# Optimization experiments

Measured on AMD Instinct MI355X. Metric: run time of the kernel, lower is better.

## Reference

```python
import jax, jax.numpy as jnp
import numpy as np

DIM = 512
EXPAND = 2
D_INNER = DIM * EXPAND            # 1024
HEADDIM = DIM * EXPAND // 8       # 128
NHEADS = D_INNER // HEADDIM       # 8
D_STATE = 128
D_CONV = 4
CONV_DIM = D_INNER + 2 * D_STATE  # 1280 (x, B, C channels)
D_IN_PROJ = 2 * D_INNER + 2 * D_STATE + NHEADS  # 2312
BSZ = 4
IMG = (16, 16, 16)                # 4096 tokens


def setup_inputs() -> dict:
    key = jax.random.key(0)
    ks = jax.random.split(key, 8)
    x = jax.random.normal(ks[0], (BSZ, DIM, *IMG), jnp.float32)
    in_proj_w = jax.random.normal(ks[1], (D_IN_PROJ, DIM), jnp.float32) * (DIM ** -0.5)
    conv_w = jax.random.normal(ks[2], (CONV_DIM, D_CONV), jnp.float32) * 0.3
    conv_b = jax.random.normal(ks[3], (CONV_DIM,), jnp.float32) * 0.1
    dt_bias = jax.random.normal(ks[4], (NHEADS,), jnp.float32) * 0.5
    A_log = jnp.log(jnp.arange(1, NHEADS + 1, dtype=jnp.float32))
    D_param = jnp.ones((NHEADS,), jnp.float32) + 0.1 * jax.random.normal(ks[5], (NHEADS,), jnp.float32)
    norm_w = jnp.ones((D_INNER,), jnp.float32)
    out_proj_w = jax.random.normal(ks[6], (DIM, D_INNER), jnp.float32) * (D_INNER ** -0.5)
    return dict(x=x, in_proj_w=in_proj_w, conv_w=conv_w, conv_b=conv_b,
                dt_bias=dt_bias, A_log=A_log, D_param=D_param,
                norm_w=norm_w, out_proj_w=out_proj_w)


def reference(x, in_proj_w, conv_w, conv_b, dt_bias, A_log, D_param, norm_w, out_proj_w):
    Bsz, C = x.shape[:2]
    img_dims = x.shape[2:]
    u = x.reshape(Bsz, C, -1).transpose(0, 2, 1)          # [b, L, d_model]
    L = u.shape[1]

    zxbcdt = jnp.einsum('bld,ed->ble', u, in_proj_w)      # [b, L, 2312]
    z = zxbcdt[..., :D_INNER]                             # gate
    xBC = zxbcdt[..., D_INNER:D_INNER + CONV_DIM]
    dt = zxbcdt[..., D_INNER + CONV_DIM:]                 # [b, L, h]
    dt = jax.nn.softplus(dt + dt_bias)

    # causal depthwise conv1d (kernel 4) + SiLU
    xp = jnp.pad(xBC, ((0, 0), (D_CONV - 1, 0), (0, 0)))
    conv = conv_b + sum(xp[:, k:k + L, :] * conv_w[:, k] for k in range(D_CONV))
    xBC = jax.nn.silu(conv)

    xs = xBC[..., :D_INNER].reshape(Bsz, L, NHEADS, HEADDIM)   # [b, L, h, p]
    Bmat = xBC[..., D_INNER:D_INNER + D_STATE]                 # [b, L, n] (ngroups=1)
    Cmat = xBC[..., D_INNER + D_STATE:]                        # [b, L, n]

    A = -jnp.exp(A_log)                                        # [h]
    dA = jnp.exp(dt * A)                                       # [b, L, h]

    def step(state, inp):
        # state: [b, h, p, n]
        x_t, B_t, C_t, dA_t, dt_t = inp
        state = state * dA_t[:, :, None, None] + \
                jnp.einsum('bhp,bn->bhpn', dt_t[:, :, None] * x_t, B_t)
        y_t = jnp.einsum('bhpn,bn->bhp', state, C_t)
        return state, y_t

    init = jnp.zeros((Bsz, NHEADS, HEADDIM, D_STATE), x.dtype)
    inputs = (xs.transpose(1, 0, 2, 3), Bmat.transpose(1, 0, 2),
              Cmat.transpose(1, 0, 2), dA.transpose(1, 0, 2), dt.transpose(1, 0, 2))
    _, ys = jax.lax.scan(step, init, inputs)                   # ys: [L, b, h, p]

    y = ys.transpose(1, 0, 2, 3) + D_param[None, None, :, None] * xs
    y = y.reshape(Bsz, L, D_INNER)

    # gated RMSNorm (norm_before_gate=False): rmsnorm(y * silu(z)) * w
    y = y * jax.nn.silu(z)
    y = y * jax.lax.rsqrt(jnp.mean(y * y, axis=-1, keepdims=True) + 1e-5) * norm_w

    out = jnp.einsum('ble,de->bld', y, out_proj_w)             # [b, L, d_model]
    out = out.transpose(0, 2, 1).reshape(Bsz, C, *img_dims)
    return out + x
```

## Files before the change

kernel.cpp:

```cpp
#include <hip/hip_runtime.h>
#include <cstdint>
#include <cstddef>

#define DIMC     512
#define D_INNER  1024
#define HEADDIM  128
#define NHEADS   8
#define D_STATE  128
#define CONV_DIM 1280
#define D_IN_PROJ 2312
#define NPAD     2432
#define BSZ      4
#define LSEQ     4096
#define BLTOT    (BSZ*LSEQ)
#define QC       64
#define NCH      (LSEQ/QC)

typedef short bf16x8 __attribute__((ext_vector_type(8)));
typedef float f32x4  __attribute__((ext_vector_type(4)));
typedef _Float16 f16x8 __attribute__((ext_vector_type(8)));
typedef _Float16 f16x4 __attribute__((ext_vector_type(4)));

__device__ inline ushort f2bf(float f) {
    uint32_t u = __float_as_uint(f);
    uint32_t r = (u + 0x7FFFu + ((u >> 16) & 1u)) >> 16;
    return (ushort)r;
}

__device__ __forceinline__ void gload_lds16(const void* g, void* l) {
    __builtin_amdgcn_global_load_lds(
        (const __attribute__((address_space(1))) void*)g,
        (__attribute__((address_space(3))) void*)l,
        16, 0, 0);
}

__global__ __launch_bounds__(256) void k0a_xT(const float* __restrict__ x, ushort* __restrict__ xT)
{
    __shared__ float t[32][33];
    const int bx = blockIdx.x;
    const int lt = bx & 127, dt = (bx >> 7) & 15, b = bx >> 11;
    const int r = threadIdx.x >> 5, c = threadIdx.x & 31;
    #pragma unroll
    for (int i = 0; i < 4; ++i) {
        int d = dt * 32 + r + i * 8;
        t[r + i * 8][c] = x[((size_t)(b * DIMC + d) << 12) + lt * 32 + c];
    }
    __syncthreads();
    #pragma unroll
    for (int i = 0; i < 4; ++i) {
        int l = lt * 32 + r + i * 8;
        xT[((size_t)(b * LSEQ + l)) * DIMC + dt * 32 + c] = f2bf(t[c][r + i * 8]);
    }
}

__global__ __launch_bounds__(256) void k0b_wb(const float* __restrict__ W, ushort* __restrict__ Wb)
{
    int i4 = (blockIdx.x * 256 + threadIdx.x) * 4;
    int e = i4 >> 9;
    ushort4 o;
    if (e < D_IN_PROJ) {
        float4 v = *(const float4*)(W + (size_t)e * DIMC + (i4 & 511));
        o.x = f2bf(v.x); o.y = f2bf(v.y); o.z = f2bf(v.z); o.w = f2bf(v.w);
    } else { o.x = o.y = o.z = o.w = 0; }
    *(ushort4*)(Wb + i4) = o;
}

__global__ __launch_bounds__(256) void k0c_wout(const float* __restrict__ W, ushort* __restrict__ Wb)
{
    int i4 = (blockIdx.x * 256 + threadIdx.x) * 4;
    float4 v = *(const float4*)(W + i4);
    ushort4 o;
    o.x = f2bf(v.x); o.y = f2bf(v.y); o.z = f2bf(v.z); o.w = f2bf(v.w);
    *(ushort4*)(Wb + i4) = o;
}

__global__ __launch_bounds__(256) void k1_mfma(
    const ushort* __restrict__ A, const ushort* __restrict__ B,
    _Float16* __restrict__ zh, _Float16* __restrict__ xbcPre,
    float* __restrict__ dtp, float* __restrict__ ldA,
    const float* __restrict__ dt_bias, const float* __restrict__ A_log)
{
    __shared__ ushort sA[128 * 64];
    __shared__ ushort sB[128 * 64];
    const int tid = threadIdx.x;
    const int lane = tid & 63;
    const int wv = tid >> 6;
    const int wm = (wv & 1) * 64, wn = (wv >> 1) * 64;
    const int m0 = blockIdx.x * 128;
    const int n0 = blockIdx.y * 128;

    f32x4 acc[4][4];
    #pragma unroll
    for (int i = 0; i < 4; ++i)
        #pragma unroll
        for (int j = 0; j < 4; ++j) acc[i][j] = (f32x4){0.f, 0.f, 0.f, 0.f};

    int rq[4], kq[4];
    #pragma unroll
    for (int q = 0; q < 4; ++q) {
        int s = q * 256 + tid;
        rq[q] = s >> 3;
        kq[q] = (s & 7) ^ (rq[q] & 7);
    }
    const int quad = lane >> 4, col = lane & 15;

    for (int kb = 0; kb < DIMC; kb += 64) {
        #pragma unroll
        for (int q = 0; q < 4; ++q)
            gload_lds16(A + (size_t)(m0 + rq[q]) * DIMC + kb + kq[q] * 8,
                        sA + (size_t)(q * 256 + wv * 64) * 8);
        #pragma unroll
        for (int q = 0; q < 4; ++q)
            gload_lds16(B + (size_t)(n0 + rq[q]) * DIMC + kb + kq[q] * 8,
                        sB + (size_t)(q * 256 + wv * 64) * 8);
        __syncthreads();
        #pragma unroll
        for (int kk = 0; kk < 2; ++kk) {
            bf16x8 af[4], bf_[4];
            #pragma unroll
            for (int mi = 0; mi < 4; ++mi) {
                int m = wm + mi * 16 + col;
                int ch = (kk * 4 + quad) ^ (m & 7);
                af[mi] = *(const bf16x8*)&sA[m * 64 + ch * 8];
            }
            #pragma unroll
            for (int ni = 0; ni < 4; ++ni) {
                int n = wn + ni * 16 + col;
                int ch = (kk * 4 + quad) ^ (n & 7);
                bf_[ni] = *(const bf16x8*)&sB[n * 64 + ch * 8];
            }
            #pragma unroll
            for (int mi = 0; mi < 4; ++mi)
                #pragma unroll
                for (int ni = 0; ni < 4; ++ni)
                    acc[mi][ni] = __builtin_amdgcn_mfma_f32_16x16x32_bf16(af[mi], bf_[ni], acc[mi][ni], 0, 0, 0);
        }
        __syncthreads();
    }

    #pragma unroll
    for (int mi = 0; mi < 4; ++mi) {
        #pragma unroll
        for (int ni = 0; ni < 4; ++ni) {
            int e = n0 + wn + ni * 16 + col;
            #pragma unroll
            for (int reg = 0; reg < 4; ++reg) {
                int m = m0 + wm + mi * 16 + quad * 4 + reg;
                float v = acc[mi][ni][reg];
                if (e < D_INNER)                  zh[(size_t)m * D_INNER + e] = (_Float16)v;
                else if (e < D_INNER + CONV_DIM)  xbcPre[(size_t)m * CONV_DIM + (e - D_INNER)] = (_Float16)v;
                else if (e < D_IN_PROJ) {
                    int h = e - (D_INNER + CONV_DIM);
                    float v0 = v + dt_bias[h];
                    float sp = (v0 > 20.f) ? v0 : log1pf(expf(v0));
                    dtp[(size_t)m * NHEADS + h] = sp;
                    ldA[(size_t)m * NHEADS + h] = sp * (-expf(A_log[h]));
                }
            }
        }
    }
}

__global__ __launch_bounds__(256) void k3x(
    const _Float16* __restrict__ xbcPre, const float* __restrict__ cw,
    const float* __restrict__ cb, _Float16* __restrict__ xsT)
{
    __shared__ _Float16 tT[32][36];
    const int bx = blockIdx.x;
    const int ct = bx & 31, tt = (bx >> 5) & 127, b = bx >> 12;
    const int t0 = tt * 32, c0 = ct * 32;
    const int tid = threadIdx.x;
    const int tq = tid >> 3, cg = tid & 7;
    const int t = t0 + tq;
    const int c = c0 + cg * 4;
    const int m = b * LSEQ + t;

    float acc[4] = {cb[c], cb[c + 1], cb[c + 2], cb[c + 3]};
    #pragma unroll
    for (int j = 0; j < 4; ++j) {
        if (t - j >= 0) {
            f16x4 xv = *(const f16x4*)&xbcPre[(size_t)(m - j) * CONV_DIM + c];
            #pragma unroll
            for (int i = 0; i < 4; ++i)
                acc[i] = fmaf((float)xv[i], cw[(c + i) * 4 + (3 - j)], acc[i]);
        }
    }
    #pragma unroll
    for (int i = 0; i < 4; ++i) {
        float s = acc[i] / (1.f + expf(-acc[i]));
        tT[cg * 4 + i][tq] = (_Float16)s;
    }
    __syncthreads();
    const int r = tid >> 3, g = tid & 7;
    f16x4 o = *(const f16x4*)&tT[r][g * 4];
    *(f16x4*)&xsT[((size_t)b * D_INNER + c0 + r) * LSEQ + t0 + g * 4] = o;
}

__global__ __launch_bounds__(256) void k3bc(
    const _Float16* __restrict__ xbcPre, const float* __restrict__ cw,
    const float* __restrict__ cb, _Float16* __restrict__ bcNat, _Float16* __restrict__ BT)
{
    __shared__ _Float16 tT[32][36];
    const int bx = blockIdx.x;
    const int ct = bx & 7, tt = (bx >> 3) & 127, b = bx >> 10;
    const int t0 = tt * 32, c0 = ct * 32;
    const int tid = threadIdx.x;
    const int tq = tid >> 3, cg = tid & 7;
    const int t = t0 + tq;
    const int ca = 1024 + c0 + cg * 4;
    const int m = b * LSEQ + t;

    float acc[4] = {cb[ca], cb[ca + 1], cb[ca + 2], cb[ca + 3]};
    #pragma unroll
    for (int j = 0; j < 4; ++j) {
        if (t - j >= 0) {
            f16x4 xv = *(const f16x4*)&xbcPre[(size_t)(m - j) * CONV_DIM + ca];
            #pragma unroll
            for (int i = 0; i < 4; ++i)
                acc[i] = fmaf((float)xv[i], cw[(ca + i) * 4 + (3 - j)], acc[i]);
        }
    }
    f16x4 nat;
    #pragma unroll
    for (int i = 0; i < 4; ++i) {
        float s = acc[i] / (1.f + expf(-acc[i]));
        nat[i] = (_Float16)s;
        tT[cg * 4 + i][tq] = nat[i];
    }
    *(f16x4*)&bcNat[(size_t)m * 256 + c0 + cg * 4] = nat;
    if (ct < 4) {
        __syncthreads();
        const int r = tid >> 3, g = tid & 7;
        f16x4 o = *(const f16x4*)&tT[r][g * 4];
        *(f16x4*)&BT[((size_t)b * D_STATE + c0 + r) * LSEQ + t0 + g * 4] = o;
    }
}

__global__ __launch_bounds__(256) void k4aA(
    const _Float16* __restrict__ xsT, const _Float16* __restrict__ BT,
    const float* __restrict__ dtp, const float* __restrict__ ldA,
    _Float16* __restrict__ ST, float* __restrict__ Pbuf)
{
    __shared__ char smem[128 * 72 * 2 * 2 + 512];
    _Float16* sXTs = (_Float16*)smem;
    _Float16* sBT  = sXTs + 128 * 72;
    float* sW = (float*)(sBT + 128 * 72);
    _Float16* sOut = sXTs;

    const int tid = threadIdx.x;
    const int lane = tid & 63;
    const int wv = tid >> 6;
    const int quad = lane >> 4, l15 = lane & 15;
    const int c = blockIdx.x & 63;
    const int h = (blockIdx.x >> 6) & 7;
    const int b = blockIdx.x >> 9;
    const int bh = b * NHEADS + h;
    const size_t mbase = (size_t)b * LSEQ + c * QC;

    if (tid < 64) {
        size_t gi = (mbase + tid) * NHEADS + h;
        float ld = ldA[gi];
        float dtv = dtp[gi];
        float cum = ld;
        #pragma unroll
        for (int off = 1; off < 64; off <<= 1) {
            float v = __shfl_up(cum, off);
            if (tid >= off) cum += v;
        }
        float cum63 = __shfl(cum, 63);
        sW[tid] = expf(cum63 - cum) * dtv;
        if (tid == 63) Pbuf[bh * NCH + c] = expf(cum63);
    }
    __syncthreads();

    #pragma unroll
    for (int k = 0; k < 4; ++k) {
        int idx = k * 256 + tid;
        int row = idx >> 3, g = idx & 7;
        int t0 = g * 8;
        f16x8 hv = *(const f16x8*)&xsT[((size_t)b * D_INNER + h * HEADDIM + row) * LSEQ + c * QC + t0];
        f16x8 sv;
        #pragma unroll
        for (int j = 0; j < 8; ++j) sv[j] = (_Float16)((float)hv[j] * sW[t0 + j]);
        *(f16x8*)&sXTs[row * 72 + t0] = sv;
        int4 bv = *(const int4*)&BT[((size_t)b * D_STATE + row) * LSEQ + c * QC + t0];
        *(int4*)&sBT[row * 72 + t0] = bv;
    }
    __syncthreads();

    f32x4 acc[2][8];
    #pragma unroll
    for (int i = 0; i < 2; ++i)
        #pragma unroll
        for (int j = 0; j < 8; ++j) acc[i][j] = (f32x4){0.f, 0.f, 0.f, 0.f};

    #pragma unroll
    for (int kk = 0; kk < 2; ++kk) {
        f16x8 af[2];
        #pragma unroll
        for (int mi = 0; mi < 2; ++mi)
            af[mi] = *(const f16x8*)&sXTs[(wv * 32 + mi * 16 + l15) * 72 + kk * 32 + quad * 8];
        #pragma unroll
        for (int ni = 0; ni < 8; ++ni) {
            f16x8 bf_ = *(const f16x8*)&sBT[(ni * 16 + l15) * 72 + kk * 32 + quad * 8];
            #pragma unroll
            for (int mi = 0; mi < 2; ++mi)
                acc[mi][ni] = __builtin_amdgcn_mfma_f32_16x16x32_f16(af[mi], bf_, acc[mi][ni], 0, 0, 0);
        }
    }
    __syncthreads();
    #pragma unroll
    for (int mi = 0; mi < 2; ++mi)
        #pragma unroll
        for (int ni = 0; ni < 8; ++ni)
            #pragma unroll
            for (int reg = 0; reg < 4; ++reg) {
                int p = wv * 32 + mi * 16 + quad * 4 + reg;
                int n = ni * 16 + l15;
                sOut[p * 136 + n] = (_Float16)acc[mi][ni][reg];
            }
    __syncthreads();
    _Float16* stg = ST + ((size_t)bh * NCH + c) * (HEADDIM * D_STATE);
    #pragma unroll
    for (int k = 0; k < 8; ++k) {
        int idx = k * 256 + tid;
        int row = idx >> 4, g = idx & 15;
        int4 v = *(const int4*)&sOut[row * 136 + g * 8];
        *(int4*)&stg[row * 128 + g * 8] = v;
    }
}

__global__ __launch_bounds__(256) void k4bB(_Float16* __restrict__ ST, const float* __restrict__ Pbuf)
{
    __shared__ float sp_[NCH];
    const int bh = blockIdx.x >> 4;
    const int seg = blockIdx.x & 15;
    const int tid = threadIdx.x;
    if (tid < NCH) sp_[tid] = Pbuf[bh * NCH + tid];
    __syncthreads();
    const int e = seg * 1024 + tid * 4;
    float r0 = 0.f, r1 = 0.f, r2 = 0.f, r3 = 0.f;
    for (int c = 0; c < NCH; ++c) {
        _Float16* ptr = ST + ((size_t)bh * NCH + c) * (HEADDIM * D_STATE) + e;
        f16x4 v = *(const f16x4*)ptr;
        float f0 = (float)v[0], f1 = (float)v[1], f2 = (float)v[2], f3 = (float)v[3];
        f16x4 o; o[0] = (_Float16)r0; o[1] = (_Float16)r1; o[2] = (_Float16)r2; o[3] = (_Float16)r3;
        *(f16x4*)ptr = o;
        float P = sp_[c];
        r0 = fmaf(r0, P, f0); r1 = fmaf(r1, P, f1);
        r2 = fmaf(r2, P, f2); r3 = fmaf(r3, P, f3);
    }
}

__global__ __launch_bounds__(256) void k4cC(
    const _Float16* __restrict__ bcNat, const _Float16* __restrict__ xsT,
    const _Float16* __restrict__ sinit, const float* __restrict__ dtp,
    const float* __restrict__ ldA, const float* __restrict__ Dp,
    _Float16* __restrict__ yB)
{
    __shared__ char smem[(64*136 + 64*136 + 128*72 + 4*16*72) * 2 + 640];
    _Float16* sC  = (_Float16*)smem;
    _Float16* sB  = sC + 64 * 136;
    _Float16* sXT = sB + 64 * 136;
    _Float16* sM  = sXT + 128 * 72;
    float* scum = (float*)(sM + 4 * 16 * 72);
    float* sdt  = scum + 64;
    _Float16* sIni = sB;
    _Float16* sY  = sC;

    const int tid = threadIdx.x;
    const int lane = tid & 63;
    const int wv = tid >> 6;
    const int quad = lane >> 4, l15 = lane & 15;
    const int c = blockIdx.x & 63;
    const int h = (blockIdx.x >> 6) & 7;
    const int b = blockIdx.x >> 9;
    const int bh = b * NHEADS + h;
    const size_t mbase = (size_t)b * LSEQ + c * QC;
    const float Dh = Dp[h];

    if (tid < 64) {
        size_t gi = (mbase + tid) * NHEADS + h;
        float ld = ldA[gi];
        float dtv = dtp[gi];
        float cum = ld;
        #pragma unroll
        for (int off = 1; off < 64; off <<= 1) {
            float v = __shfl_up(cum, off);
            if (tid >= off) cum += v;
        }
        scum[tid] = cum;
        sdt[tid] = dtv;
    }
    #pragma unroll
    for (int k = 0; k < 4; ++k) {
        int idx = k * 256 + tid;
        int t = idx >> 4, g = idx & 15;
        const _Float16* row = bcNat + (mbase + t) * 256;
        *(int4*)&sB[t * 136 + g * 8] = *(const int4*)&row[g * 8];
        *(int4*)&sC[t * 136 + g * 8] = *(const int4*)&row[128 + g * 8];
        int idx2 = k * 256 + tid;
        int p = idx2 >> 3, g2 = idx2 & 7;
        *(int4*)&sXT[p * 72 + g2 * 8] =
            *(const int4*)&xsT[((size_t)b * D_INNER + h * HEADDIM + p) * LSEQ + c * QC + g2 * 8];
    }
    __syncthreads();

    f32x4 g[4];
    #pragma unroll
    for (int j = 0; j < 4; ++j) g[j] = (f32x4){0.f, 0.f, 0.f, 0.f};
    #pragma unroll
    for (int kk = 0; kk < 4; ++kk) {
        f16x8 af = *(const f16x8*)&sC[(wv * 16 + l15) * 136 + kk * 32 + quad * 8];
        #pragma unroll
        for (int tt = 0; tt < 4; ++tt) {
            f16x8 bf_ = *(const f16x8*)&sB[(tt * 16 + l15) * 136 + kk * 32 + quad * 8];
            g[tt] = __builtin_amdgcn_mfma_f32_16x16x32_f16(af, bf_, g[tt], 0, 0, 0);
        }
    }
    _Float16* sMw = sM + wv * 16 * 72;
    #pragma unroll
    for (int tt = 0; tt < 4; ++tt) {
        int tau = tt * 16 + l15;
        #pragma unroll
        for (int reg = 0; reg < 4; ++reg) {
            int trow = quad * 4 + reg;
            int tglob = wv * 16 + trow;
            float mval;
            if (tau > tglob) mval = 0.f;
            else if (tau == tglob) mval = g[tt][reg] * sdt[tau] + Dh;
            else mval = g[tt][reg] * expf(scum[tglob] - scum[tau]) * sdt[tau];
            sMw[trow * 72 + tau] = (_Float16)mval;
        }
    }
    asm volatile("s_waitcnt lgkmcnt(0)" ::: "memory");

    f32x4 y[8];
    #pragma unroll
    for (int j = 0; j < 8; ++j) y[j] = (f32x4){0.f, 0.f, 0.f, 0.f};
    #pragma unroll
    for (int kk = 0; kk < 2; ++kk) {
        f16x8 af = *(const f16x8*)&sMw[l15 * 72 + kk * 32 + quad * 8];
        #pragma unroll
        for (int pi = 0; pi < 8; ++pi) {
            f16x8 bf_ = *(const f16x8*)&sXT[(pi * 16 + l15) * 72 + kk * 32 + quad * 8];
            y[pi] = __builtin_amdgcn_mfma_f32_16x16x32_f16(af, bf_, y[pi], 0, 0, 0);
        }
    }
    __syncthreads();
    {
        const _Float16* sg = sinit + ((size_t)bh * NCH + c) * (HEADDIM * D_STATE);
        #pragma unroll
        for (int k = 0; k < 8; ++k) {
            int idx = k * 256 + tid;
            int p = idx >> 4, gg = idx & 15;
            *(int4*)&sIni[p * 136 + gg * 8] = *(const int4*)&sg[p * 128 + gg * 8];
        }
    }
    __syncthreads();
    {
        float ea = expf(scum[wv * 16 + l15]);
        #pragma unroll
        for (int kk = 0; kk < 4; ++kk) {
            f16x8 cf = *(const f16x8*)&sC[(wv * 16 + l15) * 136 + kk * 32 + quad * 8];
            f16x8 af;
            #pragma unroll
            for (int j = 0; j < 8; ++j) af[j] = (_Float16)((float)cf[j] * ea);
            #pragma unroll
            for (int pi = 0; pi < 8; ++pi) {
                f16x8 bf_ = *(const f16x8*)&sIni[(pi * 16 + l15) * 136 + kk * 32 + quad * 8];
                y[pi] = __builtin_amdgcn_mfma_f32_16x16x32_f16(af, bf_, y[pi], 0, 0, 0);
            }
        }
    }
    __syncthreads();
    #pragma unroll
    for (int pi = 0; pi < 8; ++pi)
        #pragma unroll
        for (int reg = 0; reg < 4; ++reg) {
            int trow = wv * 16 + quad * 4 + reg;
            int p = pi * 16 + l15;
            sY[trow * 136 + p] = (_Float16)y[pi][reg];
        }
    __syncthreads();
    #pragma unroll
    for (int k = 0; k < 4; ++k) {
        int idx = k * 256 + tid;
        int t = idx >> 4, gg = idx & 15;
        int4 v = *(const int4*)&sY[t * 136 + gg * 8];
        *(int4*)&yB[(mbase + t) * D_INNER + h * HEADDIM + gg * 8] = v;
    }
}

__global__ __launch_bounds__(256) void k5_norm(
    const _Float16* __restrict__ yB, const _Float16* __restrict__ zh,
    const float* __restrict__ nw, ushort* __restrict__ ybB)
{
    const int m = blockIdx.x;
    const int tid = threadIdx.x;
    const size_t off = (size_t)m * D_INNER + tid * 4;
    f16x4 yv = *(const f16x4*)&yB[off];
    f16x4 zv = *(const f16x4*)&zh[off];
    float4 gv;
    {
        float z0 = (float)zv[0], z1 = (float)zv[1], z2 = (float)zv[2], z3 = (float)zv[3];
        gv.x = (float)yv[0] * (z0 / (1.f + expf(-z0)));
        gv.y = (float)yv[1] * (z1 / (1.f + expf(-z1)));
        gv.z = (float)yv[2] * (z2 / (1.f + expf(-z2)));
        gv.w = (float)yv[3] * (z3 / (1.f + expf(-z3)));
    }
    float ss = gv.x*gv.x + gv.y*gv.y + gv.z*gv.z + gv.w*gv.w;
    #pragma unroll
    for (int mask = 1; mask <= 32; mask <<= 1) ss += __shfl_xor(ss, mask);
    __shared__ float red[4];
    if ((tid & 63) == 0) red[tid >> 6] = ss;
    __syncthreads();
    float tot = red[0] + red[1] + red[2] + red[3];
    float scale = rsqrtf(tot * (1.f / 1024.f) + 1e-5f);
    float4 w4 = *(const float4*)(nw + tid * 4);
    ushort4 ob;
    ob.x = f2bf(gv.x * scale * w4.x);
    ob.y = f2bf(gv.y * scale * w4.y);
    ob.z = f2bf(gv.z * scale * w4.z);
    ob.w = f2bf(gv.w * scale * w4.w);
    *(ushort4*)(ybB + off) = ob;
}

__global__ __launch_bounds__(256) void k6_mfma(
    const ushort* __restrict__ A, const ushort* __restrict__ B,
    const float* __restrict__ x, float* __restrict__ out)
{
    __shared__ ushort sA[128 * 64];
    __shared__ ushort sB[128 * 64];
    const int tid = threadIdx.x;
    const int lane = tid & 63;
    const int wv = tid >> 6;
    const int wm = (wv & 1) * 64, wn = (wv >> 1) * 64;
    const int m0 = blockIdx.x * 128;
    const int n0 = blockIdx.y * 128;

    f32x4 acc[4][4];
    #pragma unroll
    for (int i = 0; i < 4; ++i)
        #pragma unroll
        for (int j = 0; j < 4; ++j) acc[i][j] = (f32x4){0.f, 0.f, 0.f, 0.f};

    int rq[4], kq[4];
    #pragma unroll
    for (int q = 0; q < 4; ++q) {
        int s = q * 256 + tid;
        rq[q] = s >> 3;
        kq[q] = (s & 7) ^ (rq[q] & 7);
    }
    const int quad = lane >> 4, col = lane & 15;

    for (int kb = 0; kb < D_INNER; kb += 64) {
        #pragma unroll
        for (int q = 0; q < 4; ++q)
            gload_lds16(A + (size_t)(m0 + rq[q]) * D_INNER + kb + kq[q] * 8,
                        sA + (size_t)(q * 256 + wv * 64) * 8);
        #pragma unroll
        for (int q = 0; q < 4; ++q)
            gload_lds16(B + (size_t)(n0 + rq[q]) * D_INNER + kb + kq[q] * 8,
                        sB + (size_t)(q * 256 + wv * 64) * 8);
        __syncthreads();
        #pragma unroll
        for (int kk = 0; kk < 2; ++kk) {
            bf16x8 af[4], bf_[4];
            #pragma unroll
            for (int mi = 0; mi < 4; ++mi) {
                int m = wm + mi * 16 + col;
                int ch = (kk * 4 + quad) ^ (m & 7);
                af[mi] = *(const bf16x8*)&sA[m * 64 + ch * 8];
            }
            #pragma unroll
            for (int ni = 0; ni < 4; ++ni) {
                int n = wn + ni * 16 + col;
                int ch = (kk * 4 + quad) ^ (n & 7);
                bf_[ni] = *(const bf16x8*)&sB[n * 64 + ch * 8];
            }
            #pragma unroll
            for (int mi = 0; mi < 4; ++mi)
                #pragma unroll
                for (int ni = 0; ni < 4; ++ni)
                    acc[mi][ni] = __builtin_amdgcn_mfma_f32_16x16x32_bf16(af[mi], bf_[ni], acc[mi][ni], 0, 0, 0);
        }
        __syncthreads();
    }

    #pragma unroll
    for (int mi = 0; mi < 4; ++mi) {
        #pragma unroll
        for (int ni = 0; ni < 4; ++ni) {
            int mm = n0 + wn + ni * 16 + col;
            int b = mm >> 12, l = mm & 4095;
            #pragma unroll
            for (int reg = 0; reg < 4; ++reg) {
                int d = m0 + wm + mi * 16 + quad * 4 + reg;
                size_t o = ((size_t)(b * DIMC + d) << 12) + l;
                out[o] = acc[mi][ni][reg] + x[o];
            }
        }
    }
}

extern "C" void kernel_launch(void* const* d_in, const int* in_sizes, int n_in,
                              void* d_out, int out_size, void* d_ws, size_t ws_size,
                              hipStream_t stream) {
    const float* x          = (const float*)d_in[0];
    const float* in_proj_w  = (const float*)d_in[1];
    const float* conv_w     = (const float*)d_in[2];
    const float* conv_b     = (const float*)d_in[3];
    const float* dt_bias    = (const float*)d_in[4];
    const float* A_log      = (const float*)d_in[5];
    const float* D_param    = (const float*)d_in[6];
    const float* norm_w     = (const float*)d_in[7];
    const float* out_proj_w = (const float*)d_in[8];
    float* out = (float*)d_out;

    float* ws = (float*)d_ws;
    float* zbuf = ws;
    _Float16* zh = (_Float16*)zbuf;
    float* regB = zbuf + (size_t)16777216;
    _Float16* xbcPre = (_Float16*)regB;
    _Float16* yB     = (_Float16*)regB;
    float* dtb  = regB + (size_t)10485760;
    float* dtp  = dtb + 131072;
    float* ldA  = dtp + 131072;
    float* Pbuf = ldA + 131072;
    float* regD = Pbuf + 2048;
    ushort* xT_k1 = (ushort*)regD;
    ushort* Wb    = xT_k1 + (size_t)BLTOT * DIMC;
    _Float16* ST  = (_Float16*)regD;
    float* regE = regD + (size_t)16777216;
    _Float16* xsT   = (_Float16*)regE;
    _Float16* BT    = xsT + (size_t)BSZ * D_INNER * LSEQ;
    _Float16* bcNat = BT + (size_t)BSZ * D_STATE * LSEQ;
    ushort* woutB = (ushort*)zbuf;

    k0a_xT<<<dim3(8192), dim3(256), 0, stream>>>(x, xT_k1);
    k0b_wb<<<dim3(NPAD * DIMC / 1024), dim3(256), 0, stream>>>(in_proj_w, Wb);
    k1_mfma<<<dim3(128, 19), dim3(256), 0, stream>>>(xT_k1, Wb, zh, xbcPre, dtp, ldA, dt_bias, A_log);
    k3x<<<dim3(16384), dim3(256), 0, stream>>>(xbcPre, conv_w, conv_b, xsT);
    k3bc<<<dim3(4096), dim3(256), 0, stream>>>(xbcPre, conv_w, conv_b, bcNat, BT);
    k4aA<<<dim3(2048), dim3(256), 0, stream>>>(xsT, BT, dtp, ldA, ST, Pbuf);
    k4bB<<<dim3(512), dim3(256), 0, stream>>>(ST, Pbuf);
    k4cC<<<dim3(2048), dim3(256), 0, stream>>>(bcNat, xsT, ST, dtp, ldA, D_param, yB);
    k5_norm<<<dim3(BLTOT), dim3(256), 0, stream>>>(yB, zh, norm_w, (ushort*)yB);
    k0c_wout<<<dim3(512), dim3(256), 0, stream>>>(out_proj_w, woutB);
    k6_mfma<<<dim3(4, 128), dim3(256), 0, stream>>>(woutB, (ushort*)yB, x, out);
}
```

Measured before the change: 431.7 us.

## Load GEMM MFMA fragments directly from global memory with register double buffering

Both projection GEMMs (in_proj and out_proj) drop the LDS staging via global_load_lds and the block barriers. Each wave now loads its A and B bf16x8 fragments straight from global memory into registers and prefetches the next k-step while the current MFMAs run. This removes LDS traffic and __syncthreads, but tiles shared between waves are fetched redundantly from global/L2. Each lane's 16-byte loads are also strided by rows, so the accesses coalesce less well.

```diff
diff --git a/kernel.cpp b/kernel.cpp
--- a/kernel.cpp
+++ b/kernel.cpp
@@ -27,13 +27,6 @@
     return (ushort)r;
 }
 
-__device__ __forceinline__ void gload_lds16(const void* g, void* l) {
-    __builtin_amdgcn_global_load_lds(
-        (const __attribute__((address_space(1))) void*)g,
-        (__attribute__((address_space(3))) void*)l,
-        16, 0, 0);
-}
-
 __global__ __launch_bounds__(256) void k0a_xT(const float* __restrict__ x, ushort* __restrict__ xT)
 {
     __shared__ float t[32][33];
@@ -80,14 +73,21 @@
     float* __restrict__ dtp, float* __restrict__ ldA,
     const float* __restrict__ dt_bias, const float* __restrict__ A_log)
 {
-    __shared__ ushort sA[128 * 64];
-    __shared__ ushort sB[128 * 64];
     const int tid = threadIdx.x;
     const int lane = tid & 63;
     const int wv = tid >> 6;
     const int wm = (wv & 1) * 64, wn = (wv >> 1) * 64;
     const int m0 = blockIdx.x * 128;
     const int n0 = blockIdx.y * 128;
+    const int quad = lane >> 4, col = lane & 15;
+
+    const ushort* Ap[4];
+    const ushort* Bp[4];
+    #pragma unroll
+    for (int i = 0; i < 4; ++i) {
+        Ap[i] = A + (size_t)(m0 + wm + i * 16 + col) * DIMC + quad * 8;
+        Bp[i] = B + (size_t)(n0 + wn + i * 16 + col) * DIMC + quad * 8;
+    }
 
     f32x4 acc[4][4];
     #pragma unroll
@@ -95,47 +95,29 @@
         #pragma unroll
         for (int j = 0; j < 4; ++j) acc[i][j] = (f32x4){0.f, 0.f, 0.f, 0.f};
 
-    int rq[4], kq[4];
-    #pragma unroll
-    for (int q = 0; q < 4; ++q) {
-        int s = q * 256 + tid;
-        rq[q] = s >> 3;
-        kq[q] = (s & 7) ^ (rq[q] & 7);
-    }
-    const int quad = lane >> 4, col = lane & 15;
-
-    for (int kb = 0; kb < DIMC; kb += 64) {
-        #pragma unroll
-        for (int q = 0; q < 4; ++q)
-            gload_lds16(A + (size_t)(m0 + rq[q]) * DIMC + kb + kq[q] * 8,
-                        sA + (size_t)(q * 256 + wv * 64) * 8);
-        #pragma unroll
-        for (int q = 0; q < 4; ++q)
-            gload_lds16(B + (size_t)(n0 + rq[q]) * DIMC + kb + kq[q] * 8,
-                        sB + (size_t)(q * 256 + wv * 64) * 8);
-        __syncthreads();
-        #pragma unroll
-        for (int kk = 0; kk < 2; ++kk) {
-            bf16x8 af[4], bf_[4];
-            #pragma unroll
-            for (int mi = 0; mi < 4; ++mi) {
-                int m = wm + mi * 16 + col;
-                int ch = (kk * 4 + quad) ^ (m & 7);
-                af[mi] = *(const bf16x8*)&sA[m * 64 + ch * 8];
+    bf16x8 af[2][4], bf_[2][4];
+    #pragma unroll
+    for (int i = 0; i < 4; ++i) {
+        af[0][i]  = *(const bf16x8*)(Ap[i]);
+        bf_[0][i] = *(const bf16x8*)(Bp[i]);
+    }
+
+    #pragma unroll
+    for (int ks = 0; ks < 16; ++ks) {
+        const int cur = ks & 1, nxt = cur ^ 1;
+        if (ks < 15) {
+            const int off = (ks + 1) * 32;
+            #pragma unroll
+            for (int i = 0; i < 4; ++i) {
+                af[nxt][i]  = *(const bf16x8*)(Ap[i] + off);
+                bf_[nxt][i] = *(const bf16x8*)(Bp[i] + off);
             }
-            #pragma unroll
-            for (int ni = 0; ni < 4; ++ni) {
-                int n = wn + ni * 16 + col;
-                int ch = (kk * 4 + quad) ^ (n & 7);
-                bf_[ni] = *(const bf16x8*)&sB[n * 64 + ch * 8];
-            }
-            #pragma unroll
-            for (int mi = 0; mi < 4; ++mi)
-                #pragma unroll
-                for (int ni = 0; ni < 4; ++ni)
-                    acc[mi][ni] = __builtin_amdgcn_mfma_f32_16x16x32_bf16(af[mi], bf_[ni], acc[mi][ni], 0, 0, 0);
-        }
-        __syncthreads();
+        }
+        #pragma unroll
+        for (int mi = 0; mi < 4; ++mi)
+            #pragma unroll
+            for (int ni = 0; ni < 4; ++ni)
+                acc[mi][ni] = __builtin_amdgcn_mfma_f32_16x16x32_bf16(af[cur][mi], bf_[cur][ni], acc[mi][ni], 0, 0, 0);
     }
 
     #pragma unroll
@@ -530,14 +512,21 @@
     const ushort* __restrict__ A, const ushort* __restrict__ B,
     const float* __restrict__ x, float* __restrict__ out)
 {
-    __shared__ ushort sA[128 * 64];
-    __shared__ ushort sB[128 * 64];
     const int tid = threadIdx.x;
     const int lane = tid & 63;
     const int wv = tid >> 6;
     const int wm = (wv & 1) * 64, wn = (wv >> 1) * 64;
     const int m0 = blockIdx.x * 128;
     const int n0 = blockIdx.y * 128;
+    const int quad = lane >> 4, col = lane & 15;
+
+    const ushort* Ap[4];
+    const ushort* Bp[4];
+    #pragma unroll
+    for (int i = 0; i < 4; ++i) {
+        Ap[i] = A + (size_t)(m0 + wm + i * 16 + col) * D_INNER + quad * 8;
+        Bp[i] = B + (size_t)(n0 + wn + i * 16 + col) * D_INNER + quad * 8;
+    }
 
     f32x4 acc[4][4];
     #pragma unroll
@@ -545,47 +534,29 @@
         #pragma unroll
         for (int j = 0; j < 4; ++j) acc[i][j] = (f32x4){0.f, 0.f, 0.f, 0.f};
 
-    int rq[4], kq[4];
-    #pragma unroll
-    for (int q = 0; q < 4; ++q) {
-        int s = q * 256 + tid;
-        rq[q] = s >> 3;
-        kq[q] = (s & 7) ^ (rq[q] & 7);
-    }
-    const int quad = lane >> 4, col = lane & 15;
-
-    for (int kb = 0; kb < D_INNER; kb += 64) {
-        #pragma unroll
-        for (int q = 0; q < 4; ++q)
-            gload_lds16(A + (size_t)(m0 + rq[q]) * D_INNER + kb + kq[q] * 8,
-                        sA + (size_t)(q * 256 + wv * 64) * 8);
-        #pragma unroll
-        for (int q = 0; q < 4; ++q)
-            gload_lds16(B + (size_t)(n0 + rq[q]) * D_INNER + kb + kq[q] * 8,
-                        sB + (size_t)(q * 256 + wv * 64) * 8);
-        __syncthreads();
-        #pragma unroll
-        for (int kk = 0; kk < 2; ++kk) {
-            bf16x8 af[4], bf_[4];
-            #pragma unroll
-            for (int mi = 0; mi < 4; ++mi) {
-                int m = wm + mi * 16 + col;
-                int ch = (kk * 4 + quad) ^ (m & 7);
-                af[mi] = *(const bf16x8*)&sA[m * 64 + ch * 8];
+    bf16x8 af[2][4], bf_[2][4];
+    #pragma unroll
+    for (int i = 0; i < 4; ++i) {
+        af[0][i]  = *(const bf16x8*)(Ap[i]);
+        bf_[0][i] = *(const bf16x8*)(Bp[i]);
+    }
+
+    #pragma unroll
+    for (int ks = 0; ks < 32; ++ks) {
+        const int cur = ks & 1, nxt = cur ^ 1;
+        if (ks < 31) {
+            const int off = (ks + 1) * 32;
+            #pragma unroll
+            for (int i = 0; i < 4; ++i) {
+                af[nxt][i]  = *(const bf16x8*)(Ap[i] + off);
+                bf_[nxt][i] = *(const bf16x8*)(Bp[i] + off);
             }
-            #pragma unroll
-            for (int ni = 0; ni < 4; ++ni) {
-                int n = wn + ni * 16 + col;
-                int ch = (kk * 4 + quad) ^ (n & 7);
-                bf_[ni] = *(const bf16x8*)&sB[n * 64 + ch * 8];
-            }
-            #pragma unroll
-            for (int mi = 0; mi < 4; ++mi)
-                #pragma unroll
-                for (int ni = 0; ni < 4; ++ni)
-                    acc[mi][ni] = __builtin_amdgcn_mfma_f32_16x16x32_bf16(af[mi], bf_[ni], acc[mi][ni], 0, 0, 0);
-        }
-        __syncthreads();
+        }
+        #pragma unroll
+        for (int mi = 0; mi < 4; ++mi)
+            #pragma unroll
+            for (int ni = 0; ni < 4; ++ni)
+                acc[mi][ni] = __builtin_amdgcn_mfma_f32_16x16x32_bf16(af[cur][mi], bf_[cur][ni], acc[mi][ni], 0, 0, 0);
     }
 
     #pragma unroll
```

Result: slower. 560.2 us (+29.8%).
